# Optimization experiments

Hardware: AMD Instinct MI355X
Metric: run time of the kernel (lower is better)

Reference implementation:

```python
import jax, jax.numpy as jnp
import numpy as np

B, S, H = 2, 2048, 4096
NH, NKV, HD = 32, 8, 128
GROUPS = NH // NKV
THETA = 10000.0


def _rope_cos_sin(position_ids):
    # inv_freq: [HD/2]
    inv_freq = 1.0 / (THETA ** (jnp.arange(0, HD, 2, dtype=jnp.float32) / HD))
    freqs = position_ids.astype(jnp.float32)[..., None] * inv_freq  # [B,S,HD/2]
    emb = jnp.concatenate([freqs, freqs], axis=-1)  # [B,S,HD]
    return jnp.cos(emb), jnp.sin(emb)


def _rotate_half(x):
    x1, x2 = jnp.split(x, 2, axis=-1)
    return jnp.concatenate([-x2, x1], axis=-1)


def setup_inputs() -> dict:
    key = jax.random.key(0)
    k1, k2, k3, k4, k5 = jax.random.split(key, 5)
    scale = 1.0 / np.sqrt(H)
    return {
        "hidden_states": jax.random.normal(k1, (B, S, H), dtype=jnp.float32),
        "position_ids": jnp.broadcast_to(jnp.arange(S, dtype=jnp.int64), (B, S)),
        "wq": jax.random.normal(k2, (NH * HD, H), dtype=jnp.float32) * scale,
        "wk": jax.random.normal(k3, (NKV * HD, H), dtype=jnp.float32) * scale,
        "wv": jax.random.normal(k4, (NKV * HD, H), dtype=jnp.float32) * scale,
        "wo": jax.random.normal(k5, (NH * HD, H), dtype=jnp.float32) * scale,
    }


def reference(hidden_states, position_ids, wq, wk, wv, wo):
    bsz, q_len, _ = hidden_states.shape
    # projections (nn.Linear: x @ W^T)
    q = jnp.einsum('bsh,dh->bsd', hidden_states, wq).reshape(bsz, q_len, NH, HD).transpose(0, 2, 1, 3)
    k = jnp.einsum('bsh,dh->bsd', hidden_states, wk).reshape(bsz, q_len, NKV, HD).transpose(0, 2, 1, 3)
    v = jnp.einsum('bsh,dh->bsd', hidden_states, wv).reshape(bsz, q_len, NKV, HD).transpose(0, 2, 1, 3)
    # RoPE
    cos, sin = _rope_cos_sin(position_ids)  # [B,S,HD]
    cos = cos[:, None, :, :]
    sin = sin[:, None, :, :]
    q = q * cos + _rotate_half(q) * sin
    k = k * cos + _rotate_half(k) * sin
    # repeat_kv (GQA expansion)
    k = jnp.repeat(k, GROUPS, axis=1)  # [B,NH,S,HD]
    v = jnp.repeat(v, GROUPS, axis=1)
    # scores + causal mask + softmax (fp32)
    scores = jnp.einsum('bhqd,bhkd->bhqk', q, k) / jnp.sqrt(jnp.float32(HD))
    causal = jnp.tril(jnp.ones((q_len, q_len), dtype=bool))
    scores = jnp.where(causal[None, None], scores, jnp.finfo(jnp.float32).min)
    attn = jax.nn.softmax(scores.astype(jnp.float32), axis=-1).astype(q.dtype)
    # AV + output projection
    out = jnp.einsum('bhqk,bhkd->bhqd', attn, v)
    out = out.transpose(0, 2, 1, 3).reshape(bsz, q_len, NH * HD)
    return jnp.einsum('bsd,hd->bsh', out, wo)
```

## Files before the change

kernel.cpp:

```cpp
#include <hip/hip_runtime.h>
#include <hip/hip_bf16.h>

#define B_    2
#define S_    2048
#define H_    4096
#define NH_   32
#define NKV_  8
#define HD_   128
#define M_    (B_*S_)
#define QKVN_ 6144

typedef unsigned short u16;
typedef __attribute__((ext_vector_type(8))) short bf16x8;
typedef __attribute__((ext_vector_type(4))) float f32x4;

__device__ __forceinline__ u16 f2bf(float x){
  unsigned u = __builtin_bit_cast(unsigned, x);
  unsigned r = u + 0x7fffu + ((u >> 16) & 1u);
  return (u16)(r >> 16);
}
__device__ __forceinline__ float bf2f(u16 x){
  unsigned u = ((unsigned)x) << 16;
  return __builtin_bit_cast(float, u);
}

__device__ __forceinline__ void gload_lds16(const u16* g, u16* l){
  __builtin_amdgcn_global_load_lds((const __attribute__((address_space(1))) void*)g,
                                   (__attribute__((address_space(3))) void*)l,
                                   16, 0, 0);
}

__global__ __launch_bounds__(256) void cast_bf16_k(const float* __restrict__ s,
                                                   u16* __restrict__ d, int n,
                                                   float sc){
  int i = (blockIdx.x * 256 + threadIdx.x) * 4;
  int stride = gridDim.x * 256 * 4;
  for (; i < n; i += stride){
    float4 v = *(const float4*)(s + i);
    uint2 o;
    o.x = (unsigned)f2bf(v.x * sc) | ((unsigned)f2bf(v.y * sc) << 16);
    o.y = (unsigned)f2bf(v.z * sc) | ((unsigned)f2bf(v.w * sc) << 16);
    *(uint2*)(d + i) = o;
  }
}

template<typename OutT>
__global__ __launch_bounds__(512, 2) void gemm256_k(const u16* __restrict__ A,
                                                    const u16* __restrict__ Bw,
                                                    OutT* __restrict__ C,
                                                    int M, int N, int K){
  __shared__ u16 LDS[65536];
  u16* Asl = LDS;
  u16* Bsl = LDS + 32768;

  const int tid = threadIdx.x;
  const int wave = tid >> 6, lane = tid & 63;
  const int l15 = lane & 15, lhi = lane >> 4;
  const int wm = wave >> 2, wn = wave & 3;

  const int nwgx = gridDim.x;
  const int lin = blockIdx.y * nwgx + blockIdx.x;
  const int cpx = (nwgx * gridDim.y) >> 3;
  const int swz = (lin & 7) * cpx + (lin >> 3);
  const int m0 = (swz / nwgx) * 256;
  const int n0 = (swz % nwgx) * 256;

  const int NKT = K >> 5;

  const int rowInChunk = lane >> 2;
  const int srcColOff = (((lane & 3) ^ ((lane >> 3) & 3)) << 3);
  const int cA0 = wave * 2;
  const u16* Ab = A  + (size_t)m0 * K;
  const u16* Bb = Bw + (size_t)n0 * K;

  const int rAb = wm * 128 + l15;
  const int rBb = wn * 64 + l15;
  const int aoff = rAb * 32 + ((lhi ^ ((rAb >> 1) & 3)) << 3);
  const int boff = rBb * 32 + ((lhi ^ ((rBb >> 1) & 3)) << 3);

  f32x4 acc[8][4] = {};

  for (int t = 0; t < 3; ++t){
    const int k0 = t * 32;
    u16* as = Asl + t * 8192;
    u16* bs = Bsl + t * 8192;
#pragma unroll
    for (int j = 0; j < 2; ++j){
      const int c = cA0 + j;
      gload_lds16(Ab + (size_t)(c * 16 + rowInChunk) * K + k0 + srcColOff, as + c * 512);
      gload_lds16(Bb + (size_t)(c * 16 + rowInChunk) * K + k0 + srcColOff, bs + c * 512);
    }
  }
  asm volatile("s_waitcnt vmcnt(8)" ::: "memory");
  __builtin_amdgcn_s_barrier();

  for (int t = 0; t < NKT; ++t){
    const int slot = t & 3;
    int wt = t + 3; if (wt >= NKT) wt -= NKT;
    const int wslot = wt & 3;
    const int wk0 = wt * 32;
    const u16* as = Asl + slot * 8192;
    const u16* bs = Bsl + slot * 8192;
    u16* was = Asl + wslot * 8192;
    u16* wbs = Bsl + wslot * 8192;

#pragma unroll
    for (int j = 0; j < 2; ++j){
      const int c = cA0 + j;
      gload_lds16(Ab + (size_t)(c * 16 + rowInChunk) * K + wk0 + srcColOff, was + c * 512);
      gload_lds16(Bb + (size_t)(c * 16 + rowInChunk) * K + wk0 + srcColOff, wbs + c * 512);
    }

    bf16x8 af[8], bfr[4];
    bfr[0] = *(const bf16x8*)(bs + boff);
#pragma unroll
    for (int f = 0; f < 8; ++f) af[f] = *(const bf16x8*)(as + aoff + f * 512);
#pragma unroll
    for (int g = 1; g < 4; ++g) bfr[g] = *(const bf16x8*)(bs + boff + g * 512);

    __builtin_amdgcn_s_setprio(1);
#pragma unroll
    for (int g = 0; g < 4; ++g)
#pragma unroll
      for (int f = 0; f < 8; ++f)
        acc[f][g] = __builtin_amdgcn_mfma_f32_16x16x32_bf16(af[f], bfr[g], acc[f][g], 0, 0, 0);
    __builtin_amdgcn_s_setprio(0);

    asm volatile("s_waitcnt vmcnt(8)" ::: "memory");
    asm volatile("s_waitcnt lgkmcnt(0)" ::: "memory");
    __builtin_amdgcn_s_barrier();
  }

#pragma unroll
  for (int f = 0; f < 8; ++f)
#pragma unroll
    for (int g = 0; g < 4; ++g)
#pragma unroll
      for (int r = 0; r < 4; ++r){
        int row = m0 + wm * 128 + f * 16 + lhi * 4 + r;
        int col = n0 + wn * 64 + g * 16 + l15;
        float v = acc[f][g][r];
        if constexpr (sizeof(OutT) == 2) C[(size_t)row * N + col] = (OutT)f2bf(v);
        else                             C[(size_t)row * N + col] = v;
      }
}

__global__ __launch_bounds__(256) void rope40_k(u16* __restrict__ X){
  int idx = blockIdx.x * 256 + threadIdx.x;
  int d   = idx & 63;
  int t2  = idx >> 6;
  int hh  = t2 % 40;
  int row = t2 / 40;
  int s   = row & (S_ - 1);
  float inv = __expf(-(float)d * 0.14391156932f);
  float ang = (float)s * inv;
  float sn = sinf(ang), cs = cosf(ang);
  size_t base = (size_t)row * QKVN_ + hh * 128;
  float x1 = bf2f(X[base + d]), x2 = bf2f(X[base + d + 64]);
  X[base + d]      = f2bf(x1 * cs - x2 * sn);
  X[base + d + 64] = f2bf(x2 * cs + x1 * sn);
}

__global__ __launch_bounds__(256) void vtrans_k(const u16* __restrict__ QKV,
                                                u16* __restrict__ Vt){
  __shared__ u16 t[32][33];
  int bkv = blockIdx.z;
  int b = bkv >> 3, kv = bkv & 7;
  int s0 = blockIdx.y * 32, d0 = blockIdx.x * 32;
  int tx = threadIdx.x, ty = threadIdx.y;
  const u16* src = QKV + (size_t)b * S_ * QKVN_ + 5120 + kv * HD_;
#pragma unroll
  for (int i = 0; i < 4; i++)
    t[ty + i*8][tx] = src[(size_t)(s0 + ty + i*8) * QKVN_ + d0 + tx];
  __syncthreads();
  u16* dst = Vt + (size_t)bkv * HD_ * S_;
#pragma unroll
  for (int i = 0; i < 4; i++)
    dst[(size_t)(d0 + ty + i*8) * S_ + s0 + tx] = t[tx][ty + i*8];
}

__global__ __launch_bounds__(256, 2) void attn_k(const u16* __restrict__ QKV,
                                                 const u16* __restrict__ Vt,
                                                 u16* __restrict__ O){
  __shared__ u16 SM[40960];
  u16* const Ks0 = SM;
  u16* const Ks1 = SM + 8192;
  u16* const Vs0 = SM + 16384;
  u16* const Vs1 = SM + 24576;

  const int lane = threadIdx.x & 63, wave = threadIdx.x >> 6;
  const int l15 = lane & 15, lhi = lane >> 4;
  u16* const Pw = SM + 32768 + wave * 2048;

  const int b = blockIdx.z, h = blockIdx.y;
  const int kvh = h >> 2;

  const u16* Kbase = QKV + (size_t)b * S_ * QKVN_ + 4096 + kvh * HD_;
  const u16* Vb    = Vt  + (size_t)(b * NKV_ + kvh) * HD_ * S_;

  const int krow_s = lane >> 4;
  const int kg     = lane & 15;
  const int vrow_s = lane >> 3;
  const int vcol_s = ((lane & 7) ^ vrow_s) * 8;
  const int swl    = (l15 & 7) << 3;

  bf16x8 ones;
#pragma unroll
  for (int i = 0; i < 8; i++) ones[i] = (short)0x3F80;

#define STAGE(tt, kd, vd) do {                                              \
    const int tkv_ = (tt) * 64;                                             \
    _Pragma("unroll")                                                       \
    for (int j_ = 0; j_ < 4; ++j_){                                         \
      const int i_ = wave * 4 + j_;                                         \
      const int kr_ = 4 * i_ + krow_s;                                      \
      const int kc_ = ((kg ^ (kr_ & 7)) << 3);                              \
      gload_lds16(Kbase + (size_t)(tkv_ + kr_) * QKVN_ + kc_, (kd) + i_ * 512); \
      const int vr_ = 8 * i_ + vrow_s;                                      \
      gload_lds16(Vb + (size_t)vr_ * S_ + tkv_ + vcol_s, (vd) + i_ * 512);  \
    }                                                                       \
  } while (0)

  for (int jj = 0; jj < 2; ++jj){
    const int J = (jj == 0) ? (int)blockIdx.x : (15 - (int)blockIdx.x);
    const int ntiles = 2 * J + 2;
    const int qg0 = J * 128 + wave * 32;

    bf16x8 aq0[4], aq1[4];
    const size_t qb0 = ((size_t)(b * S_) + qg0 + l15) * QKVN_ + h * HD_;
#pragma unroll
    for (int kb = 0; kb < 4; kb++){
      aq0[kb] = *(const bf16x8*)(QKV + qb0 + kb * 32 + lhi * 8);
      aq1[kb] = *(const bf16x8*)(QKV + qb0 + (size_t)16 * QKVN_ + kb * 32 + lhi * 8);
    }

    f32x4 o0[8] = {}, o1[8] = {};
    f32x4 os0 = {}, os1 = {};

    STAGE(0, Ks0, Vs0);
    __syncthreads();

    for (int t = 0; t < ntiles; ++t){
      const int sel = t & 1;
      const u16* ks = sel ? Ks1 : Ks0;
      const u16* vs = sel ? Vs1 : Vs0;
      if (t + 1 < ntiles){
        u16* kd = sel ? Ks0 : Ks1;
        u16* vd = sel ? Vs0 : Vs1;
        STAGE(t + 1, kd, vd);
      }
      const int kv0 = t * 64;

      f32x4 sa0[4] = {}, sa1[4] = {};
      __builtin_amdgcn_s_setprio(1);
#pragma unroll
      for (int n = 0; n < 4; n++){
        const u16* kr = ks + (n * 16 + l15) * 128;
#pragma unroll
        for (int kb = 0; kb < 4; kb++){
          bf16x8 bk = *(const bf16x8*)(kr + ((kb * 32 + lhi * 8) ^ swl));
          sa0[n] = __builtin_amdgcn_mfma_f32_16x16x32_bf16(aq0[kb], bk, sa0[n], 0, 0, 0);
          sa1[n] = __builtin_amdgcn_mfma_f32_16x16x32_bf16(aq1[kb], bk, sa1[n], 0, 0, 0);
        }
      }
      __builtin_amdgcn_s_setprio(0);

      const bool nm0 = (kv0 + 63) > qg0;
      const bool nm1 = (kv0 + 63) > qg0 + 16;
#pragma unroll
      for (int n = 0; n < 4; n++)
#pragma unroll
        for (int r = 0; r < 4; r++){
          const int col = kv0 + n * 16 + l15;
          const int prow = lhi * 4 + r;
          float v0 = sa0[n][r];
          if (nm0 && col > qg0 + prow) v0 = -1e30f;
          float v1 = sa1[n][r];
          if (nm1 && col > qg0 + 16 + prow) v1 = -1e30f;
          const int pc = (n * 16 + l15) ^ ((prow & 7) << 3);
          Pw[prow * 64 + pc]        = f2bf(__expf(v0));
          Pw[(16 + prow) * 64 + pc] = f2bf(__expf(v1));
        }
      asm volatile("s_waitcnt lgkmcnt(0)" ::: "memory");

      bf16x8 pa0[2], pa1[2];
#pragma unroll
      for (int kb2 = 0; kb2 < 2; kb2++){
        pa0[kb2] = *(const bf16x8*)(Pw + l15 * 64        + ((kb2 * 32 + lhi * 8) ^ swl));
        pa1[kb2] = *(const bf16x8*)(Pw + (16 + l15) * 64 + ((kb2 * 32 + lhi * 8) ^ swl));
      }

      __builtin_amdgcn_s_setprio(1);
#pragma unroll
      for (int f = 0; f < 8; f++){
        const u16* vr = vs + (f * 16 + l15) * 64;
#pragma unroll
        for (int kb2 = 0; kb2 < 2; kb2++){
          bf16x8 bv = *(const bf16x8*)(vr + ((kb2 * 32 + lhi * 8) ^ swl));
          o0[f] = __builtin_amdgcn_mfma_f32_16x16x32_bf16(pa0[kb2], bv, o0[f], 0, 0, 0);
          o1[f] = __builtin_amdgcn_mfma_f32_16x16x32_bf16(pa1[kb2], bv, o1[f], 0, 0, 0);
        }
      }
#pragma unroll
      for (int kb2 = 0; kb2 < 2; kb2++){
        os0 = __builtin_amdgcn_mfma_f32_16x16x32_bf16(pa0[kb2], ones, os0, 0, 0, 0);
        os1 = __builtin_amdgcn_mfma_f32_16x16x32_bf16(pa1[kb2], ones, os1, 0, 0, 0);
      }
      __builtin_amdgcn_s_setprio(0);
      __syncthreads();
    }

    float iv0[4], iv1[4];
#pragma unroll
    for (int r = 0; r < 4; r++){ iv0[r] = 1.0f / os0[r]; iv1[r] = 1.0f / os1[r]; }
#pragma unroll
    for (int f = 0; f < 8; f++)
#pragma unroll
      for (int r = 0; r < 4; r++){
        const size_t r0 = (size_t)(b * S_ + qg0 + lhi * 4 + r) * H_ + h * HD_ + f * 16 + l15;
        O[r0]                       = f2bf(o0[f][r] * iv0[r]);
        O[r0 + (size_t)16 * H_]     = f2bf(o1[f][r] * iv1[r]);
      }
  }
#undef STAGE
}

extern "C" void kernel_launch(void* const* d_in, const int* in_sizes, int n_in,
                              void* d_out, int out_size, void* d_ws, size_t ws_size,
                              hipStream_t stream) {
  const float* hs = (const float*)d_in[0];
  const float* wq = (const float*)d_in[2];
  const float* wk = (const float*)d_in[3];
  const float* wv = (const float*)d_in[4];
  const float* wo = (const float*)d_in[5];

  u16* wsp  = (u16*)d_ws;
  u16* hsb  = wsp;
  u16* wqkv = hsb + 16777216;
  u16* wob  = wqkv + 25165824;
  u16* QKV  = wob + 16777216;
  u16* Vt   = QKV + 25165824;
  u16* Oraw = Vt + 4194304;
  float* out = (float*)d_out;

  const float SCALE = 0.08838834764831845f;

  cast_bf16_k<<<2048, 256, 0, stream>>>(hs, hsb, M_ * H_, 1.0f);
  cast_bf16_k<<<2048, 256, 0, stream>>>(wq, wqkv, NH_ * HD_ * H_, SCALE);
  cast_bf16_k<<<2048, 256, 0, stream>>>(wk, wqkv + 16777216, NKV_ * HD_ * H_, 1.0f);
  cast_bf16_k<<<2048, 256, 0, stream>>>(wv, wqkv + 20971520, NKV_ * HD_ * H_, 1.0f);
  cast_bf16_k<<<2048, 256, 0, stream>>>(wo, wob, NH_ * HD_ * H_, 1.0f);

  gemm256_k<u16><<<dim3(QKVN_ / 256, M_ / 256), 512, 0, stream>>>(hsb, wqkv, QKV, M_, QKVN_, H_);

  rope40_k<<<(B_ * S_ * 40 * 64) / 256, 256, 0, stream>>>(QKV);

  vtrans_k<<<dim3(HD_ / 32, S_ / 32, B_ * NKV_), dim3(32, 8), 0, stream>>>(QKV, Vt);

  attn_k<<<dim3(8, NH_, B_), 256, 0, stream>>>(QKV, Vt, Oraw);

  gemm256_k<float><<<dim3(H_ / 256, M_ / 256), 512, 0, stream>>>(Oraw, wob, out, M_, H_, NH_ * HD_);
}
```

Before: 554.7 us.

## Restructure bf16 GEMM into 8-phase ping-pong pipeline with K=64 tiles

Replaces the 4-slot K=32 LDS ring in the 256x256 GEMM with a 2-buffer K=64 layout and an XOR swizzle. Each K-step is split into four phases, and each phase interleaves LDS fragment reads, half-tile global-to-LDS prefetches and quarter-tile MFMA blocks between barriers. The aim is to hide global load latency and LDS reads behind MFMA work and to halve loop trip count. In exchange it adds many more barriers per iteration, and the prefetch ordering and buffer reuse are harder to keep correct.

After: 528.8 us. -4.7%, faster.

```diff
diff --git a/kernel.cpp b/kernel.cpp
--- a/kernel.cpp
+++ b/kernel.cpp
@@ -45,13 +45,13 @@
 }
 
 template<typename OutT>
-__global__ __launch_bounds__(512, 2) void gemm256_k(const u16* __restrict__ A,
-                                                    const u16* __restrict__ Bw,
-                                                    OutT* __restrict__ C,
-                                                    int M, int N, int K){
+__global__ __launch_bounds__(512, 2) void gemm8p_k(const u16* __restrict__ A,
+                                                   const u16* __restrict__ Bw,
+                                                   OutT* __restrict__ C,
+                                                   int M, int N, int K){
   __shared__ u16 LDS[65536];
-  u16* Asl = LDS;
-  u16* Bsl = LDS + 32768;
+  u16* const Ab0 = LDS;
+  u16* const Bb0 = LDS + 32768;
 
   const int tid = threadIdx.x;
   const int wave = tid >> 6, lane = tid & 63;
@@ -65,69 +65,122 @@
   const int m0 = (swz / nwgx) * 256;
   const int n0 = (swz % nwgx) * 256;
 
-  const int NKT = K >> 5;
-
-  const int rowInChunk = lane >> 2;
-  const int srcColOff = (((lane & 3) ^ ((lane >> 3) & 3)) << 3);
-  const int cA0 = wave * 2;
-  const u16* Ab = A  + (size_t)m0 * K;
-  const u16* Bb = Bw + (size_t)n0 * K;
-
-  const int rAb = wm * 128 + l15;
-  const int rBb = wn * 64 + l15;
-  const int aoff = rAb * 32 + ((lhi ^ ((rAb >> 1) & 3)) << 3);
-  const int boff = rBb * 32 + ((lhi ^ ((rBb >> 1) & 3)) << 3);
+  const int NKT = K >> 6;
+  const u16* Agl = A  + (size_t)m0 * K;
+  const u16* Bgl = Bw + (size_t)n0 * K;
+
+  const int srow = lane >> 3;
+  const int sgl  = ((lane & 7) ^ srow) * 8;
+
+#define STGA(kt, h) do {                                                     \
+    u16* d_ = Ab0 + ((kt) & 1) * 16384 + ((h) * 128 + wave * 16) * 64;       \
+    const u16* s_ = Agl + (size_t)((h) * 128 + wave * 16 + srow) * K + (kt) * 64 + sgl; \
+    gload_lds16(s_, d_);                                                     \
+    gload_lds16(s_ + (size_t)8 * K, d_ + 8 * 64);                            \
+  } while (0)
+#define STGB(kt, h) do {                                                     \
+    u16* d_ = Bb0 + ((kt) & 1) * 16384 + ((h) * 128 + wave * 16) * 64;       \
+    const u16* s_ = Bgl + (size_t)((h) * 128 + wave * 16 + srow) * K + (kt) * 64 + sgl; \
+    gload_lds16(s_, d_);                                                     \
+    gload_lds16(s_ + (size_t)8 * K, d_ + 8 * 64);                            \
+  } while (0)
+
+  const int swz8  = l15 & 7;
+  const int col0  = ((lhi)     ^ swz8) * 8;
+  const int col1  = ((4 + lhi) ^ swz8) * 8;
+  const int abase = (wm * 128 + l15) * 64;
+  const int bbase = (wn * 64  + l15) * 64;
 
   f32x4 acc[8][4] = {};
 
-  for (int t = 0; t < 3; ++t){
-    const int k0 = t * 32;
-    u16* as = Asl + t * 8192;
-    u16* bs = Bsl + t * 8192;
-#pragma unroll
-    for (int j = 0; j < 2; ++j){
-      const int c = cA0 + j;
-      gload_lds16(Ab + (size_t)(c * 16 + rowInChunk) * K + k0 + srcColOff, as + c * 512);
-      gload_lds16(Bb + (size_t)(c * 16 + rowInChunk) * K + k0 + srcColOff, bs + c * 512);
-    }
-  }
-  asm volatile("s_waitcnt vmcnt(8)" ::: "memory");
+  STGB(0, 0); STGA(0, 0); STGB(0, 1); STGA(0, 1);
+  STGB(1, 0); STGA(1, 0);
+  asm volatile("s_waitcnt vmcnt(4)" ::: "memory");
   __builtin_amdgcn_s_barrier();
 
-  for (int t = 0; t < NKT; ++t){
-    const int slot = t & 3;
-    int wt = t + 3; if (wt >= NKT) wt -= NKT;
-    const int wslot = wt & 3;
-    const int wk0 = wt * 32;
-    const u16* as = Asl + slot * 8192;
-    const u16* bs = Bsl + slot * 8192;
-    u16* was = Asl + wslot * 8192;
-    u16* wbs = Bsl + wslot * 8192;
-
-#pragma unroll
-    for (int j = 0; j < 2; ++j){
-      const int c = cA0 + j;
-      gload_lds16(Ab + (size_t)(c * 16 + rowInChunk) * K + wk0 + srcColOff, was + c * 512);
-      gload_lds16(Bb + (size_t)(c * 16 + rowInChunk) * K + wk0 + srcColOff, wbs + c * 512);
-    }
-
-    bf16x8 af[8], bfr[4];
-    bfr[0] = *(const bf16x8*)(bs + boff);
-#pragma unroll
-    for (int f = 0; f < 8; ++f) af[f] = *(const bf16x8*)(as + aoff + f * 512);
-#pragma unroll
-    for (int g = 1; g < 4; ++g) bfr[g] = *(const bf16x8*)(bs + boff + g * 512);
-
+  for (int kt = 0; kt < NKT; ++kt){
+    const int buf = kt & 1;
+    const u16* As = Ab0 + buf * 16384;
+    const u16* Bs = Bb0 + buf * 16384;
+    int kt1 = kt + 1; if (kt1 >= NKT) kt1 -= NKT;
+    int kt2 = kt + 2; if (kt2 >= NKT) kt2 -= NKT;
+
+    bf16x8 af[8], bfA[4], bfB[4];
+
+#pragma unroll
+    for (int f = 0; f < 4; ++f){
+      af[f*2]   = *(const bf16x8*)(As + abase + f * 1024 + col0);
+      af[f*2+1] = *(const bf16x8*)(As + abase + f * 1024 + col1);
+    }
+#pragma unroll
+    for (int g = 0; g < 2; ++g){
+      bfA[g*2]   = *(const bf16x8*)(Bs + bbase + g * 1024 + col0);
+      bfA[g*2+1] = *(const bf16x8*)(Bs + bbase + g * 1024 + col1);
+    }
+    STGB(kt1, 1);
+    __builtin_amdgcn_s_barrier();
+    asm volatile("s_waitcnt lgkmcnt(0)" ::: "memory");
     __builtin_amdgcn_s_setprio(1);
 #pragma unroll
-    for (int g = 0; g < 4; ++g)
-#pragma unroll
-      for (int f = 0; f < 8; ++f)
-        acc[f][g] = __builtin_amdgcn_mfma_f32_16x16x32_bf16(af[f], bfr[g], acc[f][g], 0, 0, 0);
+    for (int kk = 0; kk < 2; ++kk)
+#pragma unroll
+      for (int g = 0; g < 2; ++g)
+#pragma unroll
+        for (int f = 0; f < 4; ++f)
+          acc[f][g] = __builtin_amdgcn_mfma_f32_16x16x32_bf16(af[f*2+kk], bfA[g*2+kk], acc[f][g], 0, 0, 0);
     __builtin_amdgcn_s_setprio(0);
-
-    asm volatile("s_waitcnt vmcnt(8)" ::: "memory");
+    __builtin_amdgcn_s_barrier();
+
+#pragma unroll
+    for (int g = 0; g < 2; ++g){
+      bfB[g*2]   = *(const bf16x8*)(Bs + bbase + (2 + g) * 1024 + col0);
+      bfB[g*2+1] = *(const bf16x8*)(Bs + bbase + (2 + g) * 1024 + col1);
+    }
+    STGA(kt1, 1);
+    __builtin_amdgcn_s_barrier();
     asm volatile("s_waitcnt lgkmcnt(0)" ::: "memory");
+    __builtin_amdgcn_s_setprio(1);
+#pragma unroll
+    for (int kk = 0; kk < 2; ++kk)
+#pragma unroll
+      for (int g = 0; g < 2; ++g)
+#pragma unroll
+        for (int f = 0; f < 4; ++f)
+          acc[f][2+g] = __builtin_amdgcn_mfma_f32_16x16x32_bf16(af[f*2+kk], bfB[g*2+kk], acc[f][2+g], 0, 0, 0);
+    __builtin_amdgcn_s_setprio(0);
+    __builtin_amdgcn_s_barrier();
+
+#pragma unroll
+    for (int f = 0; f < 4; ++f){
+      af[f*2]   = *(const bf16x8*)(As + abase + (4 + f) * 1024 + col0);
+      af[f*2+1] = *(const bf16x8*)(As + abase + (4 + f) * 1024 + col1);
+    }
+    STGB(kt2, 0);
+    __builtin_amdgcn_s_barrier();
+    asm volatile("s_waitcnt lgkmcnt(0)" ::: "memory");
+    __builtin_amdgcn_s_setprio(1);
+#pragma unroll
+    for (int kk = 0; kk < 2; ++kk)
+#pragma unroll
+      for (int g = 0; g < 2; ++g)
+#pragma unroll
+        for (int f = 0; f < 4; ++f)
+          acc[4+f][g] = __builtin_amdgcn_mfma_f32_16x16x32_bf16(af[f*2+kk], bfA[g*2+kk], acc[4+f][g], 0, 0, 0);
+    __builtin_amdgcn_s_setprio(0);
+    __builtin_amdgcn_s_barrier();
+
+    STGA(kt2, 0);
+    __builtin_amdgcn_s_barrier();
+    __builtin_amdgcn_s_setprio(1);
+#pragma unroll
+    for (int kk = 0; kk < 2; ++kk)
+#pragma unroll
+      for (int g = 0; g < 2; ++g)
+#pragma unroll
+        for (int f = 0; f < 4; ++f)
+          acc[4+f][2+g] = __builtin_amdgcn_mfma_f32_16x16x32_bf16(af[f*2+kk], bfB[g*2+kk], acc[4+f][2+g], 0, 0, 0);
+    __builtin_amdgcn_s_setprio(0);
+    asm volatile("s_waitcnt vmcnt(4)" ::: "memory");
     __builtin_amdgcn_s_barrier();
   }
 
@@ -143,6 +196,8 @@
         if constexpr (sizeof(OutT) == 2) C[(size_t)row * N + col] = (OutT)f2bf(v);
         else                             C[(size_t)row * N + col] = v;
       }
+#undef STGA
+#undef STGB
 }
 
 __global__ __launch_bounds__(256) void rope40_k(u16* __restrict__ X){
@@ -351,7 +406,7 @@
   cast_bf16_k<<<2048, 256, 0, stream>>>(wv, wqkv + 20971520, NKV_ * HD_ * H_, 1.0f);
   cast_bf16_k<<<2048, 256, 0, stream>>>(wo, wob, NH_ * HD_ * H_, 1.0f);
 
-  gemm256_k<u16><<<dim3(QKVN_ / 256, M_ / 256), 512, 0, stream>>>(hsb, wqkv, QKV, M_, QKVN_, H_);
+  gemm8p_k<u16><<<dim3(QKVN_ / 256, M_ / 256), 512, 0, stream>>>(hsb, wqkv, QKV, M_, QKVN_, H_);
 
   rope40_k<<<(B_ * S_ * 40 * 64) / 256, 256, 0, stream>>>(QKV);
 
@@ -359,5 +414,5 @@
 
   attn_k<<<dim3(8, NH_, B_), 256, 0, stream>>>(QKV, Vt, Oraw);
 
-  gemm256_k<float><<<dim3(H_ / 256, M_ / 256), 512, 0, stream>>>(Oraw, wob, out, M_, H_, NH_ * HD_);
-}
+  gemm8p_k<float><<<dim3(H_ / 256, M_ / 256), 512, 0, stream>>>(Oraw, wob, out, M_, H_, NH_ * HD_);
+}
```

## Replace GEMM main loop with 8-phase ping-pong schedule over 64-wide K tiles

Applied to the files above, without the earlier changes.

Both GEMMs move from a 4-slot, 32-wide K pipeline with one barrier per step to a double-buffered 64-wide K tile. Each iteration is split into eight phases that interleave LDS fragment reads, global-to-LDS staging of quarter tiles, and MFMA blocks, with explicit barriers and vmcnt waits between them. The aim is to hide global loads and LDS reads behind MFMA work, and the new XOR swizzle is meant to avoid LDS bank conflicts. The price is many more barriers per K step and fragile hand-tuned waitcnt ordering.

Result: faster. 523.5 us (-5.6%).

```diff
diff --git a/kernel.cpp b/kernel.cpp
--- a/kernel.cpp
+++ b/kernel.cpp
@@ -44,14 +44,19 @@
   }
 }
 
+#define GBAR asm volatile("s_barrier" ::: "memory")
+#define GLG0 asm volatile("s_waitcnt lgkmcnt(0)" ::: "memory")
+#define GVM6 asm volatile("s_waitcnt vmcnt(6)" ::: "memory")
+#define GVM4 asm volatile("s_waitcnt vmcnt(4)" ::: "memory")
+
 template<typename OutT>
-__global__ __launch_bounds__(512, 2) void gemm256_k(const u16* __restrict__ A,
-                                                    const u16* __restrict__ Bw,
-                                                    OutT* __restrict__ C,
-                                                    int M, int N, int K){
+__global__ __launch_bounds__(512, 2) void gemm8p_k(const u16* __restrict__ A,
+                                                   const u16* __restrict__ Bw,
+                                                   OutT* __restrict__ C,
+                                                   int M, int N, int K){
   __shared__ u16 LDS[65536];
-  u16* Asl = LDS;
-  u16* Bsl = LDS + 32768;
+  u16* const Abuf = LDS;
+  u16* const Bbuf = LDS + 32768;
 
   const int tid = threadIdx.x;
   const int wave = tid >> 6, lane = tid & 63;
@@ -65,70 +70,97 @@
   const int m0 = (swz / nwgx) * 256;
   const int n0 = (swz % nwgx) * 256;
 
-  const int NKT = K >> 5;
-
-  const int rowInChunk = lane >> 2;
-  const int srcColOff = (((lane & 3) ^ ((lane >> 3) & 3)) << 3);
-  const int cA0 = wave * 2;
-  const u16* Ab = A  + (size_t)m0 * K;
-  const u16* Bb = Bw + (size_t)n0 * K;
-
-  const int rAb = wm * 128 + l15;
-  const int rBb = wn * 64 + l15;
-  const int aoff = rAb * 32 + ((lhi ^ ((rAb >> 1) & 3)) << 3);
-  const int boff = rBb * 32 + ((lhi ^ ((rBb >> 1) & 3)) << 3);
-
+  const int NKT = K >> 6;
+  const int NI  = NKT >> 1;
+  const u16* Agl = A  + (size_t)m0 * K;
+  const u16* Bgl = Bw + (size_t)n0 * K;
+
+  const int srow = lane >> 3;
+  const int sgl  = ((lane & 7) ^ srow) * 8;
+
+#define STG(gl, bufb, t, h) do {                                             \
+    u16* d_ = (bufb) + ((t) & 1) * 16384 + ((h) * 128 + wave * 16) * 64;     \
+    const u16* s_ = (gl) + (size_t)((h) * 128 + wave * 16 + srow) * K + (t) * 64 + sgl; \
+    gload_lds16(s_, d_);                                                     \
+    gload_lds16(s_ + (size_t)8 * K, d_ + 512);                               \
+  } while (0)
+
+  const int swz8  = l15 & 7;
+  const int col0  = ((lhi)     ^ swz8) * 8;
+  const int col1  = ((4 + lhi) ^ swz8) * 8;
+  const int abase = (wm * 128 + l15) * 64;
+  const int bbase = (wn * 64  + l15) * 64;
+
+  bf16x8 aF[8], bLo[4], bHi[4];
   f32x4 acc[8][4] = {};
 
-  for (int t = 0; t < 3; ++t){
-    const int k0 = t * 32;
-    u16* as = Asl + t * 8192;
-    u16* bs = Bsl + t * 8192;
-#pragma unroll
-    for (int j = 0; j < 2; ++j){
-      const int c = cA0 + j;
-      gload_lds16(Ab + (size_t)(c * 16 + rowInChunk) * K + k0 + srcColOff, as + c * 512);
-      gload_lds16(Bb + (size_t)(c * 16 + rowInChunk) * K + k0 + srcColOff, bs + c * 512);
-    }
-  }
-  asm volatile("s_waitcnt vmcnt(8)" ::: "memory");
-  __builtin_amdgcn_s_barrier();
-
-  for (int t = 0; t < NKT; ++t){
-    const int slot = t & 3;
-    int wt = t + 3; if (wt >= NKT) wt -= NKT;
-    const int wslot = wt & 3;
-    const int wk0 = wt * 32;
-    const u16* as = Asl + slot * 8192;
-    const u16* bs = Bsl + slot * 8192;
-    u16* was = Asl + wslot * 8192;
-    u16* wbs = Bsl + wslot * 8192;
-
-#pragma unroll
-    for (int j = 0; j < 2; ++j){
-      const int c = cA0 + j;
-      gload_lds16(Ab + (size_t)(c * 16 + rowInChunk) * K + wk0 + srcColOff, was + c * 512);
-      gload_lds16(Bb + (size_t)(c * 16 + rowInChunk) * K + wk0 + srcColOff, wbs + c * 512);
-    }
-
-    bf16x8 af[8], bfr[4];
-    bfr[0] = *(const bf16x8*)(bs + boff);
-#pragma unroll
-    for (int f = 0; f < 8; ++f) af[f] = *(const bf16x8*)(as + aoff + f * 512);
-#pragma unroll
-    for (int g = 1; g < 4; ++g) bfr[g] = *(const bf16x8*)(bs + boff + g * 512);
-
-    __builtin_amdgcn_s_setprio(1);
-#pragma unroll
-    for (int g = 0; g < 4; ++g)
-#pragma unroll
-      for (int f = 0; f < 8; ++f)
-        acc[f][g] = __builtin_amdgcn_mfma_f32_16x16x32_bf16(af[f], bfr[g], acc[f][g], 0, 0, 0);
-    __builtin_amdgcn_s_setprio(0);
-
-    asm volatile("s_waitcnt vmcnt(8)" ::: "memory");
-    asm volatile("s_waitcnt lgkmcnt(0)" ::: "memory");
-    __builtin_amdgcn_s_barrier();
+#define RDA(As, f0) do { _Pragma("unroll")                                   \
+    for (int f = 0; f < 4; ++f){                                             \
+      aF[2*f]   = *(const bf16x8*)((As) + abase + ((f0)+f) * 1024 + col0);   \
+      aF[2*f+1] = *(const bf16x8*)((As) + abase + ((f0)+f) * 1024 + col1);   \
+    } } while (0)
+#define RDB(Bs, dst, g0) do { _Pragma("unroll")                              \
+    for (int g = 0; g < 2; ++g){                                             \
+      dst[2*g]   = *(const bf16x8*)((Bs) + bbase + ((g0)+g) * 1024 + col0);  \
+      dst[2*g+1] = *(const bf16x8*)((Bs) + bbase + ((g0)+g) * 1024 + col1);  \
+    } } while (0)
+#define MF(fb, gb, bsrc) do { _Pragma("unroll")                              \
+    for (int kk = 0; kk < 2; ++kk) _Pragma("unroll")                         \
+      for (int g = 0; g < 2; ++g) _Pragma("unroll")                          \
+        for (int f = 0; f < 4; ++f)                                          \
+          acc[(fb)+f][(gb)+g] = __builtin_amdgcn_mfma_f32_16x16x32_bf16(     \
+              aF[2*f+kk], bsrc[2*g+kk], acc[(fb)+f][(gb)+g], 0, 0, 0);       \
+    } while (0)
+
+  const u16* A0s = Abuf;
+  const u16* B0s = Bbuf;
+  const u16* A1s = Abuf + 16384;
+  const u16* B1s = Bbuf + 16384;
+
+  STG(Bgl, Bbuf, 0, 0); STG(Bgl, Bbuf, 0, 1);
+  STG(Agl, Abuf, 0, 0); STG(Agl, Abuf, 0, 1);
+  STG(Bgl, Bbuf, 1, 0); STG(Bgl, Bbuf, 1, 1);
+  GVM4;
+  GBAR;
+  RDB(B0s, bLo, 0);
+
+  for (int j = 0; j < NI; ++j){
+    const int t1 = 2 * j + 1;
+    int t2 = 2 * j + 2; if (t2 >= NKT) t2 -= NKT;
+    int t3 = t2 + 1;    if (t3 >= NKT) t3 -= NKT;
+
+    RDA(A0s, 0); STG(Agl, Abuf, t1, 0);
+    GBAR; GLG0;
+    __builtin_amdgcn_s_setprio(1); MF(0, 0, bLo); __builtin_amdgcn_s_setprio(0);
+    GBAR;
+    RDB(B0s, bHi, 2); STG(Agl, Abuf, t1, 1);
+    GBAR; GLG0;
+    __builtin_amdgcn_s_setprio(1); MF(0, 2, bHi); __builtin_amdgcn_s_setprio(0);
+    GBAR;
+    RDA(A0s, 4); STG(Bgl, Bbuf, t2, 0);
+    GBAR; GLG0;
+    __builtin_amdgcn_s_setprio(1); MF(4, 0, bLo); __builtin_amdgcn_s_setprio(0);
+    GVM6; GBAR;
+    RDB(B1s, bLo, 0); STG(Bgl, Bbuf, t2, 1);
+    GBAR; GLG0;
+    __builtin_amdgcn_s_setprio(1); MF(4, 2, bHi); __builtin_amdgcn_s_setprio(0);
+    GVM4; GBAR;
+    RDA(A1s, 0); STG(Agl, Abuf, t2, 0);
+    GBAR; GLG0;
+    __builtin_amdgcn_s_setprio(1); MF(0, 0, bLo); __builtin_amdgcn_s_setprio(0);
+    GBAR;
+    RDB(B1s, bHi, 2); STG(Agl, Abuf, t2, 1);
+    GBAR; GLG0;
+    __builtin_amdgcn_s_setprio(1); MF(0, 2, bHi); __builtin_amdgcn_s_setprio(0);
+    GBAR;
+    RDA(A1s, 4); STG(Bgl, Bbuf, t3, 0);
+    GBAR; GLG0;
+    __builtin_amdgcn_s_setprio(1); MF(4, 0, bLo); __builtin_amdgcn_s_setprio(0);
+    GVM6; GBAR;
+    RDB(B0s, bLo, 0); STG(Bgl, Bbuf, t3, 1);
+    GBAR; GLG0;
+    __builtin_amdgcn_s_setprio(1); MF(4, 2, bHi); __builtin_amdgcn_s_setprio(0);
+    GVM4; GBAR;
   }
 
 #pragma unroll
@@ -143,6 +175,10 @@
         if constexpr (sizeof(OutT) == 2) C[(size_t)row * N + col] = (OutT)f2bf(v);
         else                             C[(size_t)row * N + col] = v;
       }
+#undef STG
+#undef RDA
+#undef RDB
+#undef MF
 }
 
 __global__ __launch_bounds__(256) void rope40_k(u16* __restrict__ X){
@@ -351,7 +387,7 @@
   cast_bf16_k<<<2048, 256, 0, stream>>>(wv, wqkv + 20971520, NKV_ * HD_ * H_, 1.0f);
   cast_bf16_k<<<2048, 256, 0, stream>>>(wo, wob, NH_ * HD_ * H_, 1.0f);
 
-  gemm256_k<u16><<<dim3(QKVN_ / 256, M_ / 256), 512, 0, stream>>>(hsb, wqkv, QKV, M_, QKVN_, H_);
+  gemm8p_k<u16><<<dim3(QKVN_ / 256, M_ / 256), 512, 0, stream>>>(hsb, wqkv, QKV, M_, QKVN_, H_);
 
   rope40_k<<<(B_ * S_ * 40 * 64) / 256, 256, 0, stream>>>(QKV);
 
@@ -359,5 +395,5 @@
 
   attn_k<<<dim3(8, NH_, B_), 256, 0, stream>>>(QKV, Vt, Oraw);
 
-  gemm256_k<float><<<dim3(H_ / 256, M_ / 256), 512, 0, stream>>>(Oraw, wob, out, M_, H_, NH_ * HD_);
-}
+  gemm8p_k<float><<<dim3(H_ / 256, M_ / 256), 512, 0, stream>>>(Oraw, wob, out, M_, H_, NH_ * HD_);
+}
```

## Split GEMM k-step into four barrier-separated quadrant phases interleaving loads

Applied to the files above, without the earlier changes.

Restructures the main loop of the bf16 GEMM so each 32-wide k-step runs as four sub-phases, one per 2x2 quadrant of the accumulator tile. Each phase issues one slice of the next global-to-LDS prefetch and a few LDS fragment reads, then a block of MFMAs, with barriers in between. The intent is to interleave memory traffic with matrix math across waves and spread the register load of fragments over the step. The cost is several extra workgroup barriers per k-step, which can stall waves if their phases drift apart.

Measured after the change: 549.0 us. Within noise of the previous version (-1.0%).

```diff
diff --git a/kernel.cpp b/kernel.cpp
--- a/kernel.cpp
+++ b/kernel.cpp
@@ -44,14 +44,18 @@
   }
 }
 
+#define GBAR asm volatile("s_barrier" ::: "memory")
+#define GLG0 asm volatile("s_waitcnt lgkmcnt(0)" ::: "memory")
+#define GVM8 asm volatile("s_waitcnt vmcnt(8)" ::: "memory")
+
 template<typename OutT>
-__global__ __launch_bounds__(512, 2) void gemm256_k(const u16* __restrict__ A,
-                                                    const u16* __restrict__ Bw,
-                                                    OutT* __restrict__ C,
-                                                    int M, int N, int K){
+__global__ __launch_bounds__(512, 2) void gemmr4_k(const u16* __restrict__ A,
+                                                   const u16* __restrict__ Bw,
+                                                   OutT* __restrict__ C,
+                                                   int M, int N, int K){
   __shared__ u16 LDS[65536];
-  u16* Asl = LDS;
-  u16* Bsl = LDS + 32768;
+  u16* const Asl = LDS;
+  u16* const Bsl = LDS + 32768;
 
   const int tid = threadIdx.x;
   const int wave = tid >> 6, lane = tid & 63;
@@ -66,12 +70,17 @@
   const int n0 = (swz % nwgx) * 256;
 
   const int NKT = K >> 5;
+  const u16* Agl = A  + (size_t)m0 * K;
+  const u16* Bgl = Bw + (size_t)n0 * K;
 
   const int rowInChunk = lane >> 2;
   const int srcColOff = (((lane & 3) ^ ((lane >> 3) & 3)) << 3);
   const int cA0 = wave * 2;
-  const u16* Ab = A  + (size_t)m0 * K;
-  const u16* Bb = Bw + (size_t)n0 * K;
+
+#define SA(t, j) gload_lds16(Agl + (size_t)((cA0 + (j)) * 16 + rowInChunk) * K + (t) * 32 + srcColOff, \
+                             Asl + ((t) & 3) * 8192 + (cA0 + (j)) * 512)
+#define SB(t, j) gload_lds16(Bgl + (size_t)((cA0 + (j)) * 16 + rowInChunk) * K + (t) * 32 + srcColOff, \
+                             Bsl + ((t) & 3) * 8192 + (cA0 + (j)) * 512)
 
   const int rAb = wm * 128 + l15;
   const int rBb = wn * 64 + l15;
@@ -80,55 +89,72 @@
 
   f32x4 acc[8][4] = {};
 
+#pragma unroll
   for (int t = 0; t < 3; ++t){
-    const int k0 = t * 32;
-    u16* as = Asl + t * 8192;
-    u16* bs = Bsl + t * 8192;
-#pragma unroll
-    for (int j = 0; j < 2; ++j){
-      const int c = cA0 + j;
-      gload_lds16(Ab + (size_t)(c * 16 + rowInChunk) * K + k0 + srcColOff, as + c * 512);
-      gload_lds16(Bb + (size_t)(c * 16 + rowInChunk) * K + k0 + srcColOff, bs + c * 512);
-    }
+    SA(t, 0); SA(t, 1); SB(t, 0); SB(t, 1);
   }
-  asm volatile("s_waitcnt vmcnt(8)" ::: "memory");
-  __builtin_amdgcn_s_barrier();
+  GVM8;
+  GBAR;
 
   for (int t = 0; t < NKT; ++t){
-    const int slot = t & 3;
-    int wt = t + 3; if (wt >= NKT) wt -= NKT;
-    const int wslot = wt & 3;
-    const int wk0 = wt * 32;
-    const u16* as = Asl + slot * 8192;
-    const u16* bs = Bsl + slot * 8192;
-    u16* was = Asl + wslot * 8192;
-    u16* wbs = Bsl + wslot * 8192;
-
-#pragma unroll
-    for (int j = 0; j < 2; ++j){
-      const int c = cA0 + j;
-      gload_lds16(Ab + (size_t)(c * 16 + rowInChunk) * K + wk0 + srcColOff, was + c * 512);
-      gload_lds16(Bb + (size_t)(c * 16 + rowInChunk) * K + wk0 + srcColOff, wbs + c * 512);
-    }
-
-    bf16x8 af[8], bfr[4];
-    bfr[0] = *(const bf16x8*)(bs + boff);
-#pragma unroll
-    for (int f = 0; f < 8; ++f) af[f] = *(const bf16x8*)(as + aoff + f * 512);
-#pragma unroll
-    for (int g = 1; g < 4; ++g) bfr[g] = *(const bf16x8*)(bs + boff + g * 512);
-
+    const u16* as = Asl + (t & 3) * 8192;
+    const u16* bs = Bsl + (t & 3) * 8192;
+    int t3 = t + 3; if (t3 >= NKT) t3 -= NKT;
+
+    bf16x8 aLo[4], aHi[4], bLo[2], bHi[2];
+
+#pragma unroll
+    for (int f = 0; f < 4; ++f) aLo[f] = *(const bf16x8*)(as + aoff + f * 512);
+#pragma unroll
+    for (int g = 0; g < 2; ++g) bLo[g] = *(const bf16x8*)(bs + boff + g * 512);
+    SA(t3, 0);
+    GBAR; GLG0;
     __builtin_amdgcn_s_setprio(1);
 #pragma unroll
-    for (int g = 0; g < 4; ++g)
-#pragma unroll
-      for (int f = 0; f < 8; ++f)
-        acc[f][g] = __builtin_amdgcn_mfma_f32_16x16x32_bf16(af[f], bfr[g], acc[f][g], 0, 0, 0);
+    for (int g = 0; g < 2; ++g)
+#pragma unroll
+      for (int f = 0; f < 4; ++f)
+        acc[f][g] = __builtin_amdgcn_mfma_f32_16x16x32_bf16(aLo[f], bLo[g], acc[f][g], 0, 0, 0);
     __builtin_amdgcn_s_setprio(0);
-
-    asm volatile("s_waitcnt vmcnt(8)" ::: "memory");
-    asm volatile("s_waitcnt lgkmcnt(0)" ::: "memory");
-    __builtin_amdgcn_s_barrier();
+    GBAR;
+
+#pragma unroll
+    for (int g = 0; g < 2; ++g) bHi[g] = *(const bf16x8*)(bs + boff + (2 + g) * 512);
+    SA(t3, 1);
+    GBAR; GLG0;
+    __builtin_amdgcn_s_setprio(1);
+#pragma unroll
+    for (int g = 0; g < 2; ++g)
+#pragma unroll
+      for (int f = 0; f < 4; ++f)
+        acc[f][2 + g] = __builtin_amdgcn_mfma_f32_16x16x32_bf16(aLo[f], bHi[g], acc[f][2 + g], 0, 0, 0);
+    __builtin_amdgcn_s_setprio(0);
+    GBAR;
+
+#pragma unroll
+    for (int f = 0; f < 4; ++f) aHi[f] = *(const bf16x8*)(as + aoff + (4 + f) * 512);
+    SB(t3, 0);
+    GBAR; GLG0;
+    __builtin_amdgcn_s_setprio(1);
+#pragma unroll
+    for (int g = 0; g < 2; ++g)
+#pragma unroll
+      for (int f = 0; f < 4; ++f)
+        acc[4 + f][g] = __builtin_amdgcn_mfma_f32_16x16x32_bf16(aHi[f], bLo[g], acc[4 + f][g], 0, 0, 0);
+    __builtin_amdgcn_s_setprio(0);
+    GBAR;
+
+    SB(t3, 1);
+    GBAR;
+    __builtin_amdgcn_s_setprio(1);
+#pragma unroll
+    for (int g = 0; g < 2; ++g)
+#pragma unroll
+      for (int f = 0; f < 4; ++f)
+        acc[4 + f][2 + g] = __builtin_amdgcn_mfma_f32_16x16x32_bf16(aHi[f], bHi[g], acc[4 + f][2 + g], 0, 0, 0);
+    __builtin_amdgcn_s_setprio(0);
+    GVM8;
+    GBAR;
   }
 
 #pragma unroll
@@ -143,6 +169,8 @@
         if constexpr (sizeof(OutT) == 2) C[(size_t)row * N + col] = (OutT)f2bf(v);
         else                             C[(size_t)row * N + col] = v;
       }
+#undef SA
+#undef SB
 }
 
 __global__ __launch_bounds__(256) void rope40_k(u16* __restrict__ X){
@@ -351,7 +379,7 @@
   cast_bf16_k<<<2048, 256, 0, stream>>>(wv, wqkv + 20971520, NKV_ * HD_ * H_, 1.0f);
   cast_bf16_k<<<2048, 256, 0, stream>>>(wo, wob, NH_ * HD_ * H_, 1.0f);
 
-  gemm256_k<u16><<<dim3(QKVN_ / 256, M_ / 256), 512, 0, stream>>>(hsb, wqkv, QKV, M_, QKVN_, H_);
+  gemmr4_k<u16><<<dim3(QKVN_ / 256, M_ / 256), 512, 0, stream>>>(hsb, wqkv, QKV, M_, QKVN_, H_);
 
   rope40_k<<<(B_ * S_ * 40 * 64) / 256, 256, 0, stream>>>(QKV);
 
@@ -359,5 +387,5 @@
 
   attn_k<<<dim3(8, NH_, B_), 256, 0, stream>>>(QKV, Vt, Oraw);
 
-  gemm256_k<float><<<dim3(H_ / 256, M_ / 256), 512, 0, stream>>>(Oraw, wob, out, M_, H_, NH_ * HD_);
-}
+  gemmr4_k<float><<<dim3(H_ / 256, M_ / 256), 512, 0, stream>>>(Oraw, wob, out, M_, H_, NH_ * HD_);
+}
```
